# Optimization experiments

Hardware: AMD Instinct MI355X
Metric: run time of the kernel (lower is better)

Reference implementation:

```python
import jax, jax.numpy as jnp
import numpy as np

DIM = 768      # model dim
NH = 12        # num heads
WS = 32        # window/input size (H = W = WS)
B = 8          # batch


def _relative_position_index(ws):
    # Mirrors the torch buffer construction.
    coords = np.stack(np.meshgrid(np.arange(ws), np.arange(ws), indexing='ij'))  # [2, ws, ws]
    cf = coords.reshape(2, -1)                                # [2, N]
    rel = cf[:, :, None] - cf[:, None, :]                     # [2, N, N]
    rel = rel.transpose(1, 2, 0).astype(np.int64)             # [N, N, 2]
    rel[..., 0] += ws - 1
    rel[..., 1] += ws - 1
    rel[..., 0] *= 2 * ws - 1
    return rel.sum(-1)                                        # [N, N]


def setup_inputs() -> dict:
    key = jax.random.key(0)
    ks = jax.random.split(key, 5)
    std = 0.02
    x = jax.random.normal(ks[0], (B, WS, WS, DIM), jnp.float32)
    qkv_w = jax.random.normal(ks[1], (3 * DIM, DIM), jnp.float32) * std
    q_bias = jnp.zeros((DIM,), jnp.float32)
    v_bias = jnp.zeros((DIM,), jnp.float32)
    proj_w = jax.random.normal(ks[2], (DIM, DIM), jnp.float32) * std
    proj_b = jnp.zeros((DIM,), jnp.float32)
    num_rel = (2 * WS - 1) * (2 * WS - 1) + 3
    rel_table = jax.random.normal(ks[3], (num_rel, NH), jnp.float32) * std
    rel_index = jnp.asarray(_relative_position_index(WS), jnp.int32)
    return {
        'x': x, 'qkv_w': qkv_w, 'q_bias': q_bias, 'v_bias': v_bias,
        'proj_w': proj_w, 'proj_b': proj_b, 'rel_table': rel_table,
        'rel_index': rel_index,
    }


def reference(x, qkv_w, q_bias, v_bias, proj_w, proj_b, rel_table, rel_index):
    Bb, H, W, C = x.shape
    N = H * W
    hd = C // NH
    scale = hd ** (-0.5)
    # qkv bias: [q_bias, zeros(k), v_bias]
    qkv_b = jnp.concatenate([q_bias, jnp.zeros_like(v_bias), v_bias])
    qkv = x.reshape(Bb, N, C) @ qkv_w.T + qkv_b                # [B, N, 3C]
    qkv = qkv.reshape(Bb, N, 3, NH, hd).transpose(2, 0, 3, 1, 4)  # [3, B, nh, N, hd]
    q, k, v = qkv[0] * scale, qkv[1], qkv[2]
    attn = jnp.einsum('bhqd,bhkd->bhqk', q, k)                 # [B, nh, N, N]
    bias = rel_table[rel_index.reshape(-1)].reshape(N, N, NH)  # [N, N, nh]
    bias = bias.transpose(2, 0, 1)                             # [nh, N, N]
    attn = jax.nn.softmax(attn + bias[None], axis=-1)
    out = jnp.einsum('bhqk,bhkd->bhqd', attn, v)               # [B, nh, N, hd]
    out = out.transpose(0, 2, 1, 3).reshape(Bb, H, W, C)
    return out @ proj_w.T + proj_b
```

## Files before the change

kernel.cpp:

```cpp
#include <hip/hip_runtime.h>
#include <cstdint>
#include <cstddef>

#define DIMC 768
#define NHH  12
#define NSEQ 1024
#define HD   64

#define SX  6291456
#define SW1 1769472
#define SW2 589824

#define RELN 3969
#define RELP 4032

#define NCAST ((SX + SW1 + SW2) / 2048)
#define NRELB ((NHH * RELN + 255) / 256)

typedef _Float16 f16x8 __attribute__((ext_vector_type(8)));
typedef _Float16 f16x4 __attribute__((ext_vector_type(4)));
typedef float    f32x4 __attribute__((ext_vector_type(4)));
typedef float    f32x16 __attribute__((ext_vector_type(16)));

__device__ inline void gld16(const void* g, void* l) {
  __builtin_amdgcn_global_load_lds(
      (const __attribute__((address_space(1))) void*)g,
      (__attribute__((address_space(3))) void*)l, 16, 0, 0);
}

__global__ __launch_bounds__(256) void cast_f16(
    const float* __restrict__ x, const float* __restrict__ w1,
    const float* __restrict__ w2, _Float16* __restrict__ dst,
    const float* __restrict__ rel_table, float* __restrict__ relT) {
  if (blockIdx.x >= NCAST) {
    const int g = (blockIdx.x - NCAST) * 256 + threadIdx.x;
    if (g < NHH * RELN) {
      const int h = g / RELN, idx = g - h * RELN;
      relT[h * RELP + idx] = rel_table[idx * NHH + h];
    }
    return;
  }
  const long long t = (long long)blockIdx.x * 256 + threadIdx.x;
  const long long i = t * 8;
  const float* src; long long off;
  if (i < SX) { src = x; off = i; }
  else if (i < SX + SW1) { src = w1; off = i - SX; }
  else { src = w2; off = i - (SX + SW1); }
  const float4 a = *(const float4*)(src + off);
  const float4 b = *(const float4*)(src + off + 4);
  f16x8 o;
  o[0] = (_Float16)a.x; o[1] = (_Float16)a.y; o[2] = (_Float16)a.z; o[3] = (_Float16)a.w;
  o[4] = (_Float16)b.x; o[5] = (_Float16)b.y; o[6] = (_Float16)b.z; o[7] = (_Float16)b.w;
  *(f16x8*)(dst + i) = o;
}

template <int EPI>
__global__ __launch_bounds__(256) void gemm_mfma(
    const _Float16* __restrict__ A, const _Float16* __restrict__ W,
    const float* __restrict__ b0, const float* __restrict__ b1,
    float* __restrict__ outF, _Float16* __restrict__ oq,
    _Float16* __restrict__ ok, _Float16* __restrict__ ovt) {
  __shared__ _Float16 Alds[2][128 * 32];
  __shared__ _Float16 Blds[2][128 * 32];

  const int tid = threadIdx.x;
  const int w = tid >> 6, lane = tid & 63, quad = lane >> 4, l16 = lane & 15;
  const int m0 = (blockIdx.x & 63) << 7;
  const int o0 = (blockIdx.x >> 6) << 7;
  const int wr = (w >> 1) * 64, wc = (w & 1) * 64;

  f32x4 acc[4][4];
#pragma unroll
  for (int i = 0; i < 4; i++)
#pragma unroll
    for (int j = 0; j < 4; j++) acc[i][j] = (f32x4){0.f, 0.f, 0.f, 0.f};

  const int c0 = tid, c1 = 256 + tid;
  const int r0 = c0 >> 2, cb0 = (c0 & 3) * 8;
  const int r1 = c1 >> 2, cb1 = (c1 & 3) * 8;
  const _Float16* Ap0 = A + (size_t)(m0 + r0) * DIMC + cb0;
  const _Float16* Ap1 = A + (size_t)(m0 + r1) * DIMC + cb1;
  const _Float16* Wp0 = W + (size_t)(o0 + r0) * DIMC + cb0;
  const _Float16* Wp1 = W + (size_t)(o0 + r1) * DIMC + cb1;

  auto stage = [&](int k0, int bsel) {
    gld16(Ap0 + k0, &Alds[bsel][c0 * 8]);
    gld16(Ap1 + k0, &Alds[bsel][c1 * 8]);
    gld16(Wp0 + k0, &Blds[bsel][c0 * 8]);
    gld16(Wp1 + k0, &Blds[bsel][c1 * 8]);
  };

  stage(0, 0);
  int cur = 0;

#pragma unroll 2
  for (int k0 = 0; k0 < DIMC; k0 += 32) {
    __syncthreads();
    if (k0 + 32 < DIMC) stage(k0 + 32, cur ^ 1);

    f16x8 a[4], b[4];
#pragma unroll
    for (int i = 0; i < 4; i++)
      a[i] = *(const f16x8*)&Alds[cur][(wr + i * 16 + l16) * 32 + quad * 8];
#pragma unroll
    for (int j = 0; j < 4; j++)
      b[j] = *(const f16x8*)&Blds[cur][(wc + j * 16 + l16) * 32 + quad * 8];
#pragma unroll
    for (int i = 0; i < 4; i++)
#pragma unroll
      for (int j = 0; j < 4; j++)
        acc[i][j] = __builtin_amdgcn_mfma_f32_16x16x32_f16(a[i], b[j], acc[i][j], 0, 0, 0);
    cur ^= 1;
  }

  if constexpr (EPI == 0) {
#pragma unroll
    for (int j = 0; j < 4; j++) {
      const int o = o0 + wc + j * 16 + l16;
      const int part = o / DIMC;
      const int cc = o - part * DIMC;
      const int hh = cc >> 6, d = cc & 63;
      const float badd = (part == 0) ? b0[cc] : (part == 2 ? b1[cc] : 0.f);
      if (part == 2) {
#pragma unroll
        for (int i = 0; i < 4; i++) {
          const int mb = m0 + wr + i * 16 + quad * 4;
          const int bb = mb >> 10, n0 = mb & 1023;
          f16x4 vv;
#pragma unroll
          for (int r = 0; r < 4; r++) vv[r] = (_Float16)(acc[i][j][r] + badd);
          *(f16x4*)(ovt + (((size_t)(bb * NHH + hh)) * HD + d) * NSEQ + n0) = vv;
        }
      } else {
        _Float16* dst = (part == 0) ? oq : ok;
#pragma unroll
        for (int i = 0; i < 4; i++) {
#pragma unroll
          for (int r = 0; r < 4; r++) {
            const int m = m0 + wr + i * 16 + quad * 4 + r;
            const int bb = m >> 10, n = m & 1023;
            float v = acc[i][j][r];
            if (part == 0) v = (v + badd) * 0.125f;
            dst[(((size_t)(bb * NHH + hh)) * NSEQ + n) * HD + d] = (_Float16)v;
          }
        }
      }
    }
  } else {
#pragma unroll
    for (int j = 0; j < 4; j++) {
      const int o = o0 + wc + j * 16 + l16;
      const float bo = b0[o];
#pragma unroll
      for (int i = 0; i < 4; i++) {
#pragma unroll
        for (int r = 0; r < 4; r++) {
          const int m = m0 + wr + i * 16 + quad * 4 + r;
          outF[(size_t)m * DIMC + o] = acc[i][j][r] + bo;
        }
      }
    }
  }
}

__global__ __launch_bounds__(256, 3) void flash_mfma(
    const _Float16* __restrict__ Qg, const _Float16* __restrict__ Kg,
    const _Float16* __restrict__ Vtg, const float* __restrict__ relT,
    _Float16* __restrict__ AO) {
  const int nblk = blockIdx.x;
  const int bhl = nblk % 96;
  const int qt = nblk / 96;
  const int head = bhl >> 3, b = bhl & 7;
  const int bh = b * NHH + head;
  const int tid = threadIdx.x, w = tid >> 6, lane = tid & 63;
  const int ql = lane & 31;
  const int hf = lane >> 5;

  __shared__ _Float16 Klds[2][64 * 64];
  __shared__ _Float16 Vlds[2][64 * 64];
  __shared__ __attribute__((aligned(16))) float BiasLds[2][320];

  const int qglob = qt * 128 + w * 32 + ql;
  const _Float16* Qrow = Qg + ((size_t)bh * NSEQ + qglob) * HD + hf * 8;
  f16x8 bq[4];
#pragma unroll
  for (int s = 0; s < 4; s++) bq[s] = *(const f16x8*)(Qrow + s * 16);

  f32x16 O0 = {}, O1 = {};
  float psum = 0.f;

  const _Float16* Kbase = Kg + (size_t)bh * NSEQ * HD;
  const _Float16* Vtbase = Vtg + (size_t)bh * HD * NSEQ;

  const float* relTh = relT + (size_t)head * RELP;
  const int idxb = ql + 31 - 4 * hf;

  const int vrow0 = ql, vrow1 = 32 + ql;
  const int vkey0 = (vrow0 ^ (vrow0 >> 3)) & 7;
  const int vkey1 = (vrow1 ^ (vrow1 >> 3)) & 7;

  int ks0, ks1, vs0, vs1;
  {
    int c = tid;
    int r = c >> 3, cc = c & 7, key = (r ^ (r >> 3)) & 7;
    ks0 = r * HD + (cc ^ key) * 8;
    vs0 = r * NSEQ + (cc ^ key) * 8;
    c = tid + 256;
    r = c >> 3; cc = c & 7; key = (r ^ (r >> 3)) & 7;
    ks1 = r * HD + (cc ^ key) * 8;
    vs1 = r * NSEQ + (cc ^ key) * 8;
  }

  auto stage = [&](int s, int bsel) {
    const _Float16* Ks = Kbase + (size_t)s * 64 * HD;
    const _Float16* Vs = Vtbase + s * 64;
    gld16(Ks + ks0, &Klds[bsel][tid * 8]);
    gld16(Ks + ks1, &Klds[bsel][(tid + 256) * 8]);
    gld16(Vs + vs0, &Vlds[bsel][tid * 8]);
    gld16(Vs + vs1, &Vlds[bsel][(tid + 256) * 8]);
    if (tid < 79) {
      const int dyLo = qt * 4 + 30 - 2 * s;
      gld16(relTh + dyLo * 63 + tid * 4, &BiasLds[bsel][tid * 4]);
    }
  };

  stage(0, 0);

  int cur = 0;
#pragma unroll 2
  for (int s = 0; s < 16; s++) {
    __syncthreads();
    if (s + 1 < 16) stage(s + 1, cur ^ 1);

#pragma unroll
    for (int t = 0; t < 2; t++) {
      const int arow = t * 32 + ql;
      const int akey = (arow ^ (arow >> 3)) & 7;
      f32x16 S = {};
      __builtin_amdgcn_s_setprio(1);
#pragma unroll
      for (int ss = 0; ss < 4; ss++) {
        const f16x8 ak = *(const f16x8*)&Klds[cur][((arow << 3) | ((ss * 2 + hf) ^ akey)) * 8];
        S = __builtin_amdgcn_mfma_f32_32x32x16_f16(ak, bq[ss], S, 0, 0, 0);
      }
      __builtin_amdgcn_s_setprio(0);

      const float* lb = &BiasLds[cur][(w + 1 - t) * 63 + idxb];
      unsigned int dw[8];
#pragma unroll
      for (int g = 0; g < 4; g++) {
        const float b0 = lb[-8 * g - 0];
        const float b1 = lb[-8 * g - 1];
        const float b2 = lb[-8 * g - 2];
        const float b3 = lb[-8 * g - 3];
        const float p0 = __expf(S[4 * g + 0] + b0);
        const float p1 = __expf(S[4 * g + 1] + b1);
        const float p2 = __expf(S[4 * g + 2] + b2);
        const float p3 = __expf(S[4 * g + 3] + b3);
        psum += (p0 + p1) + (p2 + p3);
        union { f16x4 h; unsigned int u[2]; } cv;
        cv.h[0] = (_Float16)p0; cv.h[1] = (_Float16)p1;
        cv.h[2] = (_Float16)p2; cv.h[3] = (_Float16)p3;
        dw[2 * g] = cv.u[0]; dw[2 * g + 1] = cv.u[1];
      }

      __builtin_amdgcn_s_setprio(1);
#pragma unroll
      for (int s2 = 0; s2 < 2; s2++) {
        const unsigned int x0 = hf ? dw[4 * s2 + 0] : dw[4 * s2 + 2];
        const unsigned int x1 = hf ? dw[4 * s2 + 1] : dw[4 * s2 + 3];
        const unsigned int y0 = (unsigned int)__shfl_xor((int)x0, 32, 64);
        const unsigned int y1 = (unsigned int)__shfl_xor((int)x1, 32, 64);
        union { unsigned int u[4]; f16x8 v; } bp;
        if (hf == 0) {
          bp.u[0] = dw[4 * s2 + 0]; bp.u[1] = dw[4 * s2 + 1];
          bp.u[2] = y0;             bp.u[3] = y1;
        } else {
          bp.u[0] = y0;             bp.u[1] = y1;
          bp.u[2] = dw[4 * s2 + 2]; bp.u[3] = dw[4 * s2 + 3];
        }
        const int kchunk = t * 4 + s2 * 2 + hf;
        const f16x8 av0 = *(const f16x8*)&Vlds[cur][((vrow0 << 3) | (kchunk ^ vkey0)) * 8];
        O0 = __builtin_amdgcn_mfma_f32_32x32x16_f16(av0, bp.v, O0, 0, 0, 0);
        const f16x8 av1 = *(const f16x8*)&Vlds[cur][((vrow1 << 3) | (kchunk ^ vkey1)) * 8];
        O1 = __builtin_amdgcn_mfma_f32_32x32x16_f16(av1, bp.v, O1, 0, 0, 0);
      }
      __builtin_amdgcn_s_setprio(0);
    }
    cur ^= 1;
  }

  psum += __shfl_xor(psum, 32, 64);
  const float inv = 1.f / psum;
  _Float16* aoRow = AO + ((size_t)(b * NSEQ + qglob)) * DIMC + head * HD;
#pragma unroll
  for (int g = 0; g < 4; g++) {
    f16x4 o0, o1;
#pragma unroll
    for (int j = 0; j < 4; j++) {
      o0[j] = (_Float16)(O0[4 * g + j] * inv);
      o1[j] = (_Float16)(O1[4 * g + j] * inv);
    }
    const int d0 = 8 * g + 4 * hf;
    *(f16x4*)(aoRow + d0) = o0;
    *(f16x4*)(aoRow + 32 + d0) = o1;
  }
}

extern "C" void kernel_launch(void* const* d_in, const int* in_sizes, int n_in,
                              void* d_out, int out_size, void* d_ws, size_t ws_size,
                              hipStream_t stream) {
  const float* x        = (const float*)d_in[0];
  const float* qkv_w    = (const float*)d_in[1];
  const float* q_bias   = (const float*)d_in[2];
  const float* v_bias   = (const float*)d_in[3];
  const float* proj_w   = (const float*)d_in[4];
  const float* proj_b   = (const float*)d_in[5];
  const float* rel_tab  = (const float*)d_in[6];
  float* out = (float*)d_out;

  const size_t NTOK = (size_t)8 * NHH * NSEQ * HD;
  _Float16* Xb     = (_Float16*)d_ws;
  _Float16* Wqkvb  = Xb + SX;
  _Float16* Wprojb = Wqkvb + SW1;
  _Float16* Qb     = Wprojb + SW2;
  _Float16* Kb     = Qb + NTOK;
  _Float16* Vt     = Kb + NTOK;
  float*    relT   = (float*)(Vt + NTOK);
  _Float16* AOb    = Xb;

  cast_f16<<<dim3(NCAST + NRELB), 256, 0, stream>>>(x, qkv_w, proj_w, Xb,
                                                    rel_tab, relT);

  gemm_mfma<0><<<dim3(64 * 18), 256, 0, stream>>>(
      Xb, Wqkvb, q_bias, v_bias, nullptr, Qb, Kb, Vt);

  flash_mfma<<<dim3(768), 256, 0, stream>>>(Qb, Kb, Vt, relT, AOb);

  gemm_mfma<1><<<dim3(64 * 6), 256, 0, stream>>>(
      AOb, Wprojb, proj_b, nullptr, out, nullptr, nullptr, nullptr);
}
```

Measured before the change: 205.1 us.

## Triple-buffer GEMM LDS pipeline with explicit vmcnt waits and XOR swizzle

The MFMA GEMM kernel moves from double-buffered to triple-buffered LDS staging, with the K loop manually unrolled by three. The single __syncthreads per step becomes an explicit s_waitcnt vmcnt(4) plus s_barrier, so two global-to-LDS loads stay in flight while MFMAs run. The 16-byte chunk position within each row is XOR-swizzled by row, on both the global load and the LDS read, to reduce LDS bank conflicts. LDS use grows by half, which could lower occupancy, and the hand-written waitcnt counts depend on each stage issuing exactly four loads.

```diff
diff --git a/kernel.cpp b/kernel.cpp
--- a/kernel.cpp
+++ b/kernel.cpp
@@ -54,20 +54,55 @@
   *(f16x8*)(dst + i) = o;
 }
 
+#define GSTAGE(K0, TGT)                               \
+  {                                                   \
+    const int kk = (K0);                              \
+    gld16(Ap0 + kk, &Alds[TGT][c0 * 8]);              \
+    gld16(Ap1 + kk, &Alds[TGT][c1 * 8]);              \
+    gld16(Wp0 + kk, &Blds[TGT][c0 * 8]);              \
+    gld16(Wp1 + kk, &Blds[TGT][c1 * 8]);              \
+  }
+
+#define GCOMP(CUR)                                                             \
+  {                                                                            \
+    f16x8 a[4], b[4];                                                          \
+    _Pragma("unroll") for (int i = 0; i < 4; i++)                              \
+      a[i] = *(const f16x8*)&Alds[CUR][(wr + i * 16 + l16) * 32 + rchunk * 8]; \
+    _Pragma("unroll") for (int j = 0; j < 4; j++)                              \
+      b[j] = *(const f16x8*)&Blds[CUR][(wc + j * 16 + l16) * 32 + rchunk * 8]; \
+    _Pragma("unroll") for (int i = 0; i < 4; i++)                              \
+      _Pragma("unroll") for (int j = 0; j < 4; j++)                            \
+        acc[i][j] =                                                            \
+            __builtin_amdgcn_mfma_f32_16x16x32_f16(a[i], b[j], acc[i][j], 0, 0, 0); \
+  }
+
+#define GSYNC4                                        \
+  __builtin_amdgcn_sched_barrier(0);                  \
+  asm volatile("s_waitcnt vmcnt(4)" ::: "memory");    \
+  __builtin_amdgcn_s_barrier();                       \
+  __builtin_amdgcn_sched_barrier(0);
+
+#define GSYNC0                                        \
+  __builtin_amdgcn_sched_barrier(0);                  \
+  asm volatile("s_waitcnt vmcnt(0)" ::: "memory");    \
+  __builtin_amdgcn_s_barrier();                       \
+  __builtin_amdgcn_sched_barrier(0);
+
 template <int EPI>
 __global__ __launch_bounds__(256) void gemm_mfma(
     const _Float16* __restrict__ A, const _Float16* __restrict__ W,
     const float* __restrict__ b0, const float* __restrict__ b1,
     float* __restrict__ outF, _Float16* __restrict__ oq,
     _Float16* __restrict__ ok, _Float16* __restrict__ ovt) {
-  __shared__ _Float16 Alds[2][128 * 32];
-  __shared__ _Float16 Blds[2][128 * 32];
+  __shared__ _Float16 Alds[3][128 * 32];
+  __shared__ _Float16 Blds[3][128 * 32];
 
   const int tid = threadIdx.x;
   const int w = tid >> 6, lane = tid & 63, quad = lane >> 4, l16 = lane & 15;
   const int m0 = (blockIdx.x & 63) << 7;
   const int o0 = (blockIdx.x >> 6) << 7;
   const int wr = (w >> 1) * 64, wc = (w & 1) * 64;
+  const int rchunk = quad ^ ((l16 >> 1) & 3);
 
   f32x4 acc[4][4];
 #pragma unroll
@@ -76,41 +111,28 @@
     for (int j = 0; j < 4; j++) acc[i][j] = (f32x4){0.f, 0.f, 0.f, 0.f};
 
   const int c0 = tid, c1 = 256 + tid;
-  const int r0 = c0 >> 2, cb0 = (c0 & 3) * 8;
-  const int r1 = c1 >> 2, cb1 = (c1 & 3) * 8;
-  const _Float16* Ap0 = A + (size_t)(m0 + r0) * DIMC + cb0;
-  const _Float16* Ap1 = A + (size_t)(m0 + r1) * DIMC + cb1;
-  const _Float16* Wp0 = W + (size_t)(o0 + r0) * DIMC + cb0;
-  const _Float16* Wp1 = W + (size_t)(o0 + r1) * DIMC + cb1;
-
-  auto stage = [&](int k0, int bsel) {
-    gld16(Ap0 + k0, &Alds[bsel][c0 * 8]);
-    gld16(Ap1 + k0, &Alds[bsel][c1 * 8]);
-    gld16(Wp0 + k0, &Blds[bsel][c0 * 8]);
-    gld16(Wp1 + k0, &Blds[bsel][c1 * 8]);
-  };
-
-  stage(0, 0);
-  int cur = 0;
-
-#pragma unroll 2
-  for (int k0 = 0; k0 < DIMC; k0 += 32) {
-    __syncthreads();
-    if (k0 + 32 < DIMC) stage(k0 + 32, cur ^ 1);
-
-    f16x8 a[4], b[4];
-#pragma unroll
-    for (int i = 0; i < 4; i++)
-      a[i] = *(const f16x8*)&Alds[cur][(wr + i * 16 + l16) * 32 + quad * 8];
-#pragma unroll
-    for (int j = 0; j < 4; j++)
-      b[j] = *(const f16x8*)&Blds[cur][(wc + j * 16 + l16) * 32 + quad * 8];
-#pragma unroll
-    for (int i = 0; i < 4; i++)
-#pragma unroll
-      for (int j = 0; j < 4; j++)
-        acc[i][j] = __builtin_amdgcn_mfma_f32_16x16x32_f16(a[i], b[j], acc[i][j], 0, 0, 0);
-    cur ^= 1;
+  const int r0 = c0 >> 2, r1 = c1 >> 2;
+  const int g0 = ((c0 & 3) ^ ((r0 >> 1) & 3)) * 8;
+  const int g1 = ((c1 & 3) ^ ((r1 >> 1) & 3)) * 8;
+  const _Float16* Ap0 = A + (size_t)(m0 + r0) * DIMC + g0;
+  const _Float16* Ap1 = A + (size_t)(m0 + r1) * DIMC + g1;
+  const _Float16* Wp0 = W + (size_t)(o0 + r0) * DIMC + g0;
+  const _Float16* Wp1 = W + (size_t)(o0 + r1) * DIMC + g1;
+
+  GSTAGE(0, 0);
+  GSTAGE(32, 1);
+
+  for (int sb = 0; sb < 24; sb += 3) {
+    GSYNC4;
+    if (sb + 2 < 24) GSTAGE((sb + 2) * 32, 2);
+    GCOMP(0);
+    GSYNC4;
+    if (sb + 3 < 24) GSTAGE((sb + 3) * 32, 0);
+    GCOMP(1);
+    if (sb + 2 == 23) { GSYNC0; }
+    else              { GSYNC4; }
+    if (sb + 4 < 24) GSTAGE((sb + 4) * 32, 1);
+    GCOMP(2);
   }
 
   if constexpr (EPI == 0) {
```

Result: slower. 211.9 us (+3.3%).
